# Optimization experiments

Measured on AMD Instinct MI355X. Metric: run time of the kernel, lower is better.

The kernel has to match this reference:

```python
import jax, jax.numpy as jnp
import numpy as np

B, N, C, NH = 4, 2304, 256, 8
HD = C // NH            # head dim = 32
HS = WS = 48            # H = W = sqrt(N)
RADIUS = 3.0
MLP_HID = 4 * C
SCALE = HD ** (-0.5)
NEG = -1e9              # stands in for -inf (identical softmax up to fp eps)
EPS = 1e-6


def spatial_mask():
    # get_spatial_mask: cdist of (y, x) grid coords, -inf where dist > radius
    yy, xx = jnp.meshgrid(jnp.arange(HS), jnp.arange(WS), indexing='ij')
    coords = jnp.stack([yy, xx], -1).reshape(-1, 2).astype(jnp.float32)  # [N, 2]
    d2 = jnp.sum((coords[:, None, :] - coords[None, :, :]) ** 2, -1)     # [N, N]
    return jnp.where(d2 > RADIUS * RADIUS, NEG, 0.0)


def layernorm(x, g, b):
    mu = jnp.mean(x, -1, keepdims=True)
    var = jnp.mean((x - mu) ** 2, -1, keepdims=True)
    return (x - mu) * jax.lax.rsqrt(var + EPS) * g + b


def setup_inputs() -> dict:
    key = jax.random.key(0)
    ks = jax.random.split(key, 16)
    s = 0.02
    return {
        'x':    jax.random.normal(ks[0], (B, N, C), jnp.float32),
        'x_kv': jax.random.normal(ks[1], (B, N, C), jnp.float32),
        'Wq': jax.random.normal(ks[2], (C, C), jnp.float32) * s,
        'bq': jnp.zeros((C,), jnp.float32),
        'Wk': jax.random.normal(ks[3], (C, C), jnp.float32) * s,
        'bk': jnp.zeros((C,), jnp.float32),
        'Wv': jax.random.normal(ks[4], (C, C), jnp.float32) * s,
        'bv': jnp.zeros((C,), jnp.float32),
        'Wp': jax.random.normal(ks[5], (C, C), jnp.float32) * s,
        'bp': jnp.zeros((C,), jnp.float32),
        'g1': jnp.ones((C,), jnp.float32),
        'b1': jnp.zeros((C,), jnp.float32),
        'g2': jnp.ones((C,), jnp.float32),
        'b2': jnp.zeros((C,), jnp.float32),
        'W1': jax.random.normal(ks[6], (C, MLP_HID), jnp.float32) * s,
        'bm1': jnp.zeros((MLP_HID,), jnp.float32),
        'W2': jax.random.normal(ks[7], (MLP_HID, C), jnp.float32) * s,
        'bm2': jnp.zeros((C,), jnp.float32),
    }


def reference(x, x_kv, Wq, bq, Wk, bk, Wv, bv, Wp, bp,
              g1, b1, g2, b2, W1, bm1, W2, bm2):
    mask = spatial_mask()                                  # [N, N]
    h = layernorm(x, g1, b1)
    hkv = layernorm(x_kv, g1, b1)
    q = (h @ Wq + bq).reshape(B, N, NH, HD)
    k = (hkv @ Wk + bk).reshape(B, N, NH, HD)
    v = (hkv @ Wv + bv).reshape(B, N, NH, HD)
    scores = jnp.einsum('bqhd,bkhd->bhqk', q, k) * SCALE + mask
    attn = jax.nn.softmax(scores, axis=-1)
    out = jnp.einsum('bhqk,bkhd->bqhd', attn, v).reshape(B, N, C)
    x = x + out @ Wp + bp
    m = layernorm(x, g2, b2)
    x = x + jax.nn.gelu(m @ W1 + bm1, approximate=False) @ W2 + bm2
    return x
```

## Files before the change

### kernel.cpp

```cpp
#include <hip/hip_runtime.h>
#include <hip/hip_fp16.h>
#include <math.h>

#define BB 4
#define NN 2304
#define CC 256
#define HS 48
#define HID 1024
#define BNROWS (BB * NN)
#define ATTN_SCALE 0.17677669529663687f

typedef _Float16 f16;
typedef __attribute__((ext_vector_type(2))) _Float16 h2;
typedef __attribute__((ext_vector_type(8))) _Float16 h8;
typedef __attribute__((ext_vector_type(4))) float f4;

#define GLLS16(g, l)                                                        \
    __builtin_amdgcn_global_load_lds(                                       \
        (const __attribute__((address_space(1))) unsigned int*)(g),         \
        (__attribute__((address_space(3))) unsigned int*)(l), 16, 0, 0)
#define WAIT_VM0()   asm volatile("s_waitcnt vmcnt(0)" ::: "memory")
#define WAIT_VM2()   asm volatile("s_waitcnt vmcnt(2)" ::: "memory")
#define WAIT_VM4()   asm volatile("s_waitcnt vmcnt(4)" ::: "memory")
#define WAIT_VM5()   asm volatile("s_waitcnt vmcnt(5)" ::: "memory")
#define WAIT_VM6()   asm volatile("s_waitcnt vmcnt(6)" ::: "memory")
#define WAIT_LGKM0() asm volatile("s_waitcnt lgkmcnt(0)" ::: "memory")

static __device__ __forceinline__ float wave_sum64(float v) {
    v += __shfl_xor(v, 32, 64);
    v += __shfl_xor(v, 16, 64);
    v += __shfl_xor(v, 8, 64);
    v += __shfl_xor(v, 4, 64);
    v += __shfl_xor(v, 2, 64);
    v += __shfl_xor(v, 1, 64);
    return v;
}

static __device__ __forceinline__ int xcd_swizzle_lin() {
    const int gx = (int)gridDim.x;
    const int lin = (int)blockIdx.y * gx + (int)blockIdx.x;
    const int nwg = gx * (int)gridDim.y;
    return (nwg & 7) ? lin : ((lin & 7) * (nwg >> 3) + (lin >> 3));
}

__global__ __launch_bounds__(256) void prep_ln1_kernel(
    const float* __restrict__ x, const float* __restrict__ xkv,
    const float* __restrict__ Wq, const float* __restrict__ Wk,
    const float* __restrict__ Wv, const float* __restrict__ Wp,
    const float* __restrict__ W1, const float* __restrict__ W2,
    const float* __restrict__ bq, const float* __restrict__ bk,
    const float* __restrict__ bv,
    const float* __restrict__ g, const float* __restrict__ be,
    f16* __restrict__ WqkvT, f16* __restrict__ WpT,
    f16* __restrict__ W1T, f16* __restrict__ W2T, float* __restrict__ bqkv,
    f16* __restrict__ hq, f16* __restrict__ hkv)
{
    __shared__ float tt[32][33];
    int bx = blockIdx.x;
    const int tid = threadIdx.x;
    if (bx < 768) {
        const float* src; f16* dst; int K, N;
        if (bx < 64)        { src = Wq; dst = WqkvT;           K = 256;  N = 256; }
        else if (bx < 128)  { src = Wk; dst = WqkvT + 65536;   K = 256;  N = 256;  bx -= 64; }
        else if (bx < 192)  { src = Wv; dst = WqkvT + 131072;  K = 256;  N = 256;  bx -= 128; }
        else if (bx < 256)  { src = Wp; dst = WpT;             K = 256;  N = 256;  bx -= 192; }
        else if (bx < 512)  { src = W1; dst = W1T;             K = 256;  N = 1024; bx -= 256; }
        else                { src = W2; dst = W2T;             K = 1024; N = 256;  bx -= 512; }
        const int tN = N >> 5;
        const int kt = bx / tN, nt = bx - kt * tN;
        const int rr = tid >> 5, cc = tid & 31;
#pragma unroll
        for (int j = 0; j < 4; ++j)
            tt[rr + 8 * j][cc] = src[(size_t)(kt * 32 + rr + 8 * j) * N + nt * 32 + cc];
        __syncthreads();
#pragma unroll
        for (int j = 0; j < 4; ++j)
            dst[(size_t)(nt * 32 + rr + 8 * j) * K + kt * 32 + cc] = (f16)tt[cc][rr + 8 * j];
        return;
    }
    if (bx == 768) {
        if (tid < 256) {
            bqkv[tid]       = bq[tid];
            bqkv[tid + 256] = bk[tid];
            bqkv[tid + 512] = bv[tid];
        }
        return;
    }
    const int r = (bx - 769) * 4 + (tid >> 6);
    const int lane = tid & 63;
    const float* src; f16* dst;
    if (r < BNROWS) { src = x + (size_t)r * CC;              dst = hq + (size_t)r * CC; }
    else { src = xkv + (size_t)(r - BNROWS) * CC; dst = hkv + (size_t)(r - BNROWS) * CC; }
    const float4 v = ((const float4*)src)[lane];
    const float mu = wave_sum64(v.x + v.y + v.z + v.w) * (1.0f / CC);
    const float d0 = v.x - mu, d1 = v.y - mu, d2 = v.z - mu, d3 = v.w - mu;
    const float var = wave_sum64(d0 * d0 + d1 * d1 + d2 * d2 + d3 * d3) * (1.0f / CC);
    const float rs = rsqrtf(var + 1e-6f);
    const float4 g4 = ((const float4*)g)[lane];
    const float4 b4 = ((const float4*)be)[lane];
    h2 o01 = (h2){(f16)(d0 * rs * g4.x + b4.x), (f16)(d1 * rs * g4.y + b4.y)};
    h2 o23 = (h2){(f16)(d2 * rs * g4.z + b4.z), (f16)(d3 * rs * g4.w + b4.w)};
    ((h2*)dst)[lane * 2] = o01;
    ((h2*)dst)[lane * 2 + 1] = o23;
}

template <bool QKV>
__global__ __launch_bounds__(256, 4) void gemm_wave(
    const f16* __restrict__ Aq, const f16* __restrict__ Akv,
    const f16* __restrict__ Bt, const float* __restrict__ bias,
    void* __restrict__ out1, void* __restrict__ outkv, int N, int K)
{
    __shared__ f16 lds[4 * 6144];
    const int tid = threadIdx.x;
    const int wid = tid >> 6, lane = tid & 63;
    const int ln15 = lane & 15, quad = lane >> 4;
    const int jr = lane >> 2, js = lane & 3;
    f16* slot = lds + wid * 6144;
    const int sl = xcd_swizzle_lin();
    const int gx = (int)gridDim.x;
    const int bx = sl % gx, by = sl / gx;
    const int n0 = bx * 64;
    const int m0 = (by * 4 + wid) * 32;
    const f16* Ap = QKV ? (n0 < 256 ? Aq : Akv) : Aq;

    size_t ga[2], gb[4];
#pragma unroll
    for (int i = 0; i < 2; ++i) {
        const int r = i * 16 + jr;
        const int q = (js - (r >> 1)) & 3;
        ga[i] = (size_t)(m0 + r) * K + q * 8;
    }
#pragma unroll
    for (int i = 0; i < 4; ++i) {
        const int r = i * 16 + jr;
        const int q = (js - (r >> 1)) & 3;
        gb[i] = (size_t)(n0 + r) * K + q * 8;
    }
    int aoff[2], boff[4];
#pragma unroll
    for (int mt = 0; mt < 2; ++mt) {
        const int r = mt * 16 + ln15;
        aoff[mt] = (r * 4 + ((quad + (r >> 1)) & 3)) * 16;
    }
#pragma unroll
    for (int nt = 0; nt < 4; ++nt) {
        const int r = nt * 16 + ln15;
        boff[nt] = (r * 4 + ((quad + (r >> 1)) & 3)) * 16;
    }

    f4 acc[2][4];
#pragma unroll
    for (int i = 0; i < 2; ++i)
#pragma unroll
        for (int j = 0; j < 4; ++j) acc[i][j] = (f4){0.f, 0.f, 0.f, 0.f};

    {
        f16* Al = slot;
        f16* Bl = slot + 1024;
#pragma unroll
        for (int i = 0; i < 2; ++i) GLLS16(Ap + ga[i], Al + i * 512);
#pragma unroll
        for (int i = 0; i < 4; ++i) GLLS16(Bt + gb[i], Bl + i * 512);
    }

    int cur = 0;
    for (int k0 = 0; k0 < K; k0 += 32) {
        const bool more = (k0 + 32 < K);
        f16* Ac = slot + cur * 3072;
        f16* Bc = Ac + 1024;
        if (more) {
            f16* An = slot + (cur ^ 1) * 3072;
            f16* Bn = An + 1024;
            WAIT_LGKM0();
#pragma unroll
            for (int i = 0; i < 2; ++i) GLLS16(Ap + ga[i] + k0 + 32, An + i * 512);
#pragma unroll
            for (int i = 0; i < 4; ++i) GLLS16(Bt + gb[i] + k0 + 32, Bn + i * 512);
            WAIT_VM6();
        } else {
            WAIT_VM0();
        }
        h8 aF[2], bF[4];
#pragma unroll
        for (int nt = 0; nt < 4; ++nt)
            bF[nt] = *(const h8*)((const char*)Bc + boff[nt]);
#pragma unroll
        for (int mt = 0; mt < 2; ++mt)
            aF[mt] = *(const h8*)((const char*)Ac + aoff[mt]);
#pragma unroll
        for (int mt = 0; mt < 2; ++mt)
#pragma unroll
            for (int nt = 0; nt < 4; ++nt)
                acc[mt][nt] = __builtin_amdgcn_mfma_f32_16x16x32_f16(
                    aF[mt], bF[nt], acc[mt][nt], 0, 0, 0);
        cur ^= 1;
    }

    f16* qdst = nullptr; int qstr = 0, qn0 = 0;
    if (QKV) {
        if (n0 < 256) { qdst = (f16*)out1;  qstr = 256; qn0 = n0; }
        else          { qdst = (f16*)outkv; qstr = 512; qn0 = n0 - 256; }
    }
#pragma unroll
    for (int nt = 0; nt < 4; ++nt) {
        const int gn = n0 + nt * 16 + ln15;
        const float bs = bias[gn];
#pragma unroll
        for (int mt = 0; mt < 2; ++mt) {
#pragma unroll
            for (int r = 0; r < 4; ++r) {
                const int gm = m0 + mt * 16 + quad * 4 + r;
                float v = acc[mt][nt][r] + bs;
                if (QKV) {
                    qdst[(size_t)gm * qstr + qn0 + nt * 16 + ln15] = (f16)v;
                } else {
                    ((f16*)out1)[(size_t)gm * N + gn] = (f16)v;
                }
            }
        }
    }
}

__global__ __launch_bounds__(256, 4) void gemm_op_ln2(
    const f16* __restrict__ Aa, const f16* __restrict__ Bt,
    const float* __restrict__ bias, const float* __restrict__ xres,
    const float* __restrict__ g, const float* __restrict__ be,
    f16* __restrict__ x1, f16* __restrict__ m2)
{
    __shared__ f16 lds[4 * 5120];
    __shared__ float sred[16][4][2];
    const int tid = threadIdx.x;
    const int wid = tid >> 6, lane = tid & 63;
    const int ln15 = lane & 15, quad = lane >> 4;
    const int jr = lane >> 2, js = lane & 3;
    f16* slot = lds + wid * 5120;
    const int m0 = blockIdx.x * 16;
    const int n0 = wid * 64;
    const int K = 256;

    size_t ga, gb[4];
    {
        const int q = (js - (jr >> 1)) & 3;
        ga = (size_t)(m0 + jr) * K + q * 8;
    }
#pragma unroll
    for (int i = 0; i < 4; ++i) {
        const int r = i * 16 + jr;
        const int q = (js - (r >> 1)) & 3;
        gb[i] = (size_t)(n0 + r) * K + q * 8;
    }
    const int aoff = (ln15 * 4 + ((quad + (ln15 >> 1)) & 3)) * 16;
    int boff[4];
#pragma unroll
    for (int nt = 0; nt < 4; ++nt) {
        const int r = nt * 16 + ln15;
        boff[nt] = (r * 4 + ((quad + (r >> 1)) & 3)) * 16;
    }

    f4 acc[4];
#pragma unroll
    for (int j = 0; j < 4; ++j) acc[j] = (f4){0.f, 0.f, 0.f, 0.f};

    {
        f16* Al = slot;
        f16* Bl = slot + 512;
        GLLS16(Aa + ga, Al);
#pragma unroll
        for (int i = 0; i < 4; ++i) GLLS16(Bt + gb[i], Bl + i * 512);
    }
    int cur = 0;
    for (int k0 = 0; k0 < K; k0 += 32) {
        const bool more = (k0 + 32 < K);
        f16* Ac = slot + cur * 2560;
        f16* Bc = Ac + 512;
        if (more) {
            f16* An = slot + (cur ^ 1) * 2560;
            f16* Bn = An + 512;
            WAIT_LGKM0();
            GLLS16(Aa + ga + k0 + 32, An);
#pragma unroll
            for (int i = 0; i < 4; ++i) GLLS16(Bt + gb[i] + k0 + 32, Bn + i * 512);
            WAIT_VM5();
        } else {
            WAIT_VM0();
        }
        h8 aF, bF[4];
#pragma unroll
        for (int nt = 0; nt < 4; ++nt)
            bF[nt] = *(const h8*)((const char*)Bc + boff[nt]);
        aF = *(const h8*)((const char*)Ac + aoff);
#pragma unroll
        for (int nt = 0; nt < 4; ++nt)
            acc[nt] = __builtin_amdgcn_mfma_f32_16x16x32_f16(
                aF, bF[nt], acc[nt], 0, 0, 0);
        cur ^= 1;
    }

    float bsv[4], g2v[4], b2v[4];
#pragma unroll
    for (int nt = 0; nt < 4; ++nt) {
        const int gn = n0 + nt * 16 + ln15;
        bsv[nt] = bias[gn];
        g2v[nt] = g[gn];
        b2v[nt] = be[gn];
    }
    float s1[4], s2[4];
#pragma unroll
    for (int r = 0; r < 4; ++r) { s1[r] = 0.f; s2[r] = 0.f; }
#pragma unroll
    for (int r = 0; r < 4; ++r) {
        const int gm = m0 + quad * 4 + r;
#pragma unroll
        for (int nt = 0; nt < 4; ++nt) {
            const int gn = n0 + nt * 16 + ln15;
            float v = acc[nt][r] + bsv[nt] + xres[(size_t)gm * CC + gn];
            acc[nt][r] = v;
            x1[(size_t)gm * CC + gn] = (f16)v;
            s1[r] += v;
            s2[r] += v * v;
        }
    }
#pragma unroll
    for (int off = 1; off < 16; off <<= 1) {
#pragma unroll
        for (int r = 0; r < 4; ++r) {
            s1[r] += __shfl_xor(s1[r], off, 64);
            s2[r] += __shfl_xor(s2[r], off, 64);
        }
    }
    if (ln15 == 0) {
#pragma unroll
        for (int r = 0; r < 4; ++r) {
            const int rr = quad * 4 + r;
            sred[rr][wid][0] = s1[r];
            sred[rr][wid][1] = s2[r];
        }
    }
    __syncthreads();
#pragma unroll
    for (int r = 0; r < 4; ++r) {
        const int rr = quad * 4 + r;
        const int gm = m0 + rr;
        float a = 0.f, b = 0.f;
#pragma unroll
        for (int w = 0; w < 4; ++w) {
            a += sred[rr][w][0];
            b += sred[rr][w][1];
        }
        const float mu = a * (1.0f / CC);
        const float var = fmaxf(b * (1.0f / CC) - mu * mu, 0.0f);
        const float rs = rsqrtf(var + 1e-6f);
#pragma unroll
        for (int nt = 0; nt < 4; ++nt) {
            const int gn = n0 + nt * 16 + ln15;
            const float v = acc[nt][r];
            m2[(size_t)gm * CC + gn] = (f16)((v - mu) * rs * g2v[nt] + b2v[nt]);
        }
    }
}

template <int BM, int BN, int WGM, int WGN, bool GELU, bool FINAL>
__global__ __launch_bounds__(256, 2) void gemm_pipe(
    const f16* __restrict__ A, const f16* __restrict__ Bt,
    const float* __restrict__ bias, const f16* __restrict__ resid16,
    void* __restrict__ outv, int N, int K)
{
    constexpr int A_G = BM / 16, B_G = BN / 16, T = A_G + B_G;
    constexpr int L = T / 4;
    constexpr int BUFE = (BM + BN) * 32;
    constexpr int WM = BM / WGM, WN = BN / WGN;
    constexpr int MT = WM / 16;
    static_assert(WN == 64, "epilogue assumes 4 n-frags of 16");
    static_assert(T % 4 == 0, "stage loads divide across 4 waves");
    __shared__ f16 lds[3 * BUFE];
    const int tid = threadIdx.x;
    const int wid = tid >> 6, lane = tid & 63;
    const int ln15 = lane & 15, quad = lane >> 4;
    const int jr = lane >> 2, js = lane & 3;
    const int wr = wid / WGN, wc = wid % WGN;

    const int sl = xcd_swizzle_lin();
    const int gx = (int)gridDim.x;
    const int m0 = (sl % gx) * BM;
    const int n0 = (sl / gx) * BN;

    const size_t gabase = (size_t)jr * K + (size_t)(((js - (jr >> 1)) & 3) * 8);

    int aoff[MT], boff[4];
#pragma unroll
    for (int mt = 0; mt < MT; ++mt) {
        const int rr = wr * WM + mt * 16 + ln15;
        aoff[mt] = (rr * 4 + ((quad + (rr >> 1)) & 3)) * 16;
    }
#pragma unroll
    for (int nt = 0; nt < 4; ++nt) {
        const int rr = wc * WN + nt * 16 + ln15;
        boff[nt] = BM * 64 + (rr * 4 + ((quad + (rr >> 1)) & 3)) * 16;
    }

    f4 acc[MT][4];
#pragma unroll
    for (int i = 0; i < MT; ++i)
#pragma unroll
        for (int j = 0; j < 4; ++j) acc[i][j] = (f4){0.f, 0.f, 0.f, 0.f};

#define GP_STAGE(dst, kk)                                                     \
    _Pragma("unroll")                                                         \
    for (int i = 0; i < L; ++i) {                                             \
        const int g = wid + i * 4;                                            \
        const f16* base;                                                      \
        int dofs;                                                             \
        if (g < A_G) {                                                        \
            base = A + (size_t)(m0 + g * 16) * K;                             \
            dofs = g * 512;                                                   \
        } else {                                                              \
            base = Bt + (size_t)(n0 + (g - A_G) * 16) * K;                    \
            dofs = BM * 32 + (g - A_G) * 512;                                 \
        }                                                                     \
        GLLS16(base + gabase + (kk), (dst) + dofs);                           \
    }

    GP_STAGE(lds, 0);
    GP_STAGE(lds + BUFE, 32);

    const int nst = K >> 5;
    for (int s = 0; s < nst; ++s) {
        if (s + 1 < nst) {
            if constexpr (L == 4) { WAIT_VM4(); } else { WAIT_VM2(); }
        } else {
            WAIT_VM0();
        }
        __builtin_amdgcn_s_barrier();
        __builtin_amdgcn_sched_barrier(0);
        if (s + 2 < nst) { GP_STAGE(lds + ((s + 2) % 3) * BUFE, (s + 2) * 32); }
        f16* bufc = lds + (s % 3) * BUFE;
        h8 aF[MT], bF[4];
#pragma unroll
        for (int nt = 0; nt < 4; ++nt)
            bF[nt] = *(const h8*)((const char*)bufc + boff[nt]);
#pragma unroll
        for (int mt = 0; mt < MT; ++mt)
            aF[mt] = *(const h8*)((const char*)bufc + aoff[mt]);
        __builtin_amdgcn_s_setprio(1);
#pragma unroll
        for (int mt = 0; mt < MT; ++mt)
#pragma unroll
            for (int nt = 0; nt < 4; ++nt)
                acc[mt][nt] = __builtin_amdgcn_mfma_f32_16x16x32_f16(
                    aF[mt], bF[nt], acc[mt][nt], 0, 0, 0);
        __builtin_amdgcn_s_setprio(0);
    }
#undef GP_STAGE

#pragma unroll
    for (int nt = 0; nt < 4; ++nt) {
        const int gn = n0 + wc * WN + nt * 16 + ln15;
        const float bs = bias[gn];
#pragma unroll
        for (int mt = 0; mt < MT; ++mt) {
#pragma unroll
            for (int r = 0; r < 4; ++r) {
                const int gm = m0 + wr * WM + mt * 16 + quad * 4 + r;
                float v = acc[mt][nt][r] + bs;
                if (GELU) v = 0.5f * v * (1.0f + erff(v * 0.70710678118654752f));
                if (FINAL) {
                    v += (float)resid16[(size_t)gm * N + gn];
                    ((float*)outv)[(size_t)gm * N + gn] = v;
                } else {
                    ((f16*)outv)[(size_t)gm * N + gn] = (f16)v;
                }
            }
        }
    }
}

__device__ __constant__ int ATT_DY[29] = {
    -3, -2, -2, -2, -2, -2, -1, -1, -1, -1, -1, 0, 0, 0, 0,
    0, 0, 0, 1, 1, 1, 1, 1, 2, 2, 2, 2, 2, 3};
__device__ __constant__ int ATT_DX[29] = {
    0, -2, -1, 0, 1, 2, -2, -1, 0, 1, 2, -3, -2, -1, 0,
    1, 2, 3, -2, -1, 0, 1, 2, -2, -1, 0, 1, 2, 0};

__global__ __launch_bounds__(128) void attn_tile_kernel(
    const f16* __restrict__ qf, const f16* __restrict__ kvf,
    f16* __restrict__ ao)
{
    __shared__ f16 ks[196][66];
    __shared__ f16 vs[196][66];
    const int tile = blockIdx.x, hp = blockIdx.y, b = blockIdx.z;
    const int ty0 = (tile / 6) * 8, tx0 = (tile - (tile / 6) * 6) * 8;
    const int tid = threadIdx.x;

    const int q = tid & 63, hh = tid >> 6;
    const int qy = q >> 3, qx = q & 7;
    const size_t qrow = (size_t)b * NN + (ty0 + qy) * HS + tx0 + qx;
    const f16* qp = qf + qrow * CC + hp * 64 + hh * 32;
    uint4 qa[4];
#pragma unroll
    for (int i = 0; i < 4; ++i) qa[i] = ((const uint4*)qp)[i];

#pragma unroll
    for (int bt = 0; bt < 5; ++bt) {
        uint4 v[5];
        int rr[5], sg[5];
#pragma unroll
        for (int j = 0; j < 5; ++j) {
            const int it = bt * 5 + j;
            const int idx = tid + it * 128;
            const int r = idx >> 4, seg = idx & 15;
            rr[j] = r; sg[j] = seg;
            const int ry = r / 14;
            const int gy = ty0 - 3 + ry, gx = tx0 - 3 + (r - ry * 14);
            uint4 val = {0u, 0u, 0u, 0u};
            const bool act = (it < 24) || (tid < 64);
            if (act && (unsigned)gy < HS && (unsigned)gx < HS) {
                const size_t rowb = ((size_t)b * NN + gy * HS + gx) * 512;
                const int ch = (seg < 8) ? (hp * 64 + seg * 8)
                                         : (256 + hp * 64 + (seg - 8) * 8);
                val = *(const uint4*)&kvf[rowb + ch];
            }
            v[j] = val;
        }
#pragma unroll
        for (int j = 0; j < 5; ++j) {
            const int it = bt * 5 + j;
            if (it == 24 && tid >= 64) continue;
            f16* dstp = (sg[j] < 8) ? &ks[rr[j]][(sg[j] & 7) * 8]
                                    : &vs[rr[j]][(sg[j] & 7) * 8];
            ((unsigned int*)dstp)[0] = v[j].x;
            ((unsigned int*)dstp)[1] = v[j].y;
            ((unsigned int*)dstp)[2] = v[j].z;
            ((unsigned int*)dstp)[3] = v[j].w;
        }
    }
    __syncthreads();

    const h2* q2 = (const h2*)qa;

    float s[29];
#pragma unroll
    for (int n = 0; n < 29; ++n) {
        const int dy = ATT_DY[n], dx = ATT_DX[n];
        const int r = (qy + 3 + dy) * 14 + qx + 3 + dx;
        const bool valid = (unsigned)(ty0 + qy + dy) < HS &&
                           (unsigned)(tx0 + qx + dx) < HS;
        float a = 0.0f;
        const h2* kp = (const h2*)&ks[r][hh * 32];
#pragma unroll
        for (int i = 0; i < 16; ++i)
            a = __builtin_amdgcn_fdot2(q2[i], kp[i], a, false);
        s[n] = valid ? a * ATTN_SCALE : -1e30f;
    }
    float m = s[0];
#pragma unroll
    for (int n = 1; n < 29; ++n) m = fmaxf(m, s[n]);
    float l = 0.0f;
#pragma unroll
    for (int n = 0; n < 29; ++n) { s[n] = __expf(s[n] - m); l += s[n]; }
    h2 a2[16];
#pragma unroll
    for (int i = 0; i < 16; ++i) a2[i] = (h2){(f16)0.f, (f16)0.f};
#pragma unroll
    for (int n = 0; n < 29; ++n) {
        const int dy = ATT_DY[n], dx = ATT_DX[n];
        const int r = (qy + 3 + dy) * 14 + qx + 3 + dx;
        const f16 pn = (f16)s[n];
        const h2 ph = (h2){pn, pn};
        const h2* vp = (const h2*)&vs[r][hh * 32];
#pragma unroll
        for (int i = 0; i < 16; ++i) a2[i] += ph * vp[i];
    }
    const float inv = 1.0f / l;
    uint4 ov[4];
    f16* oh = (f16*)ov;
#pragma unroll
    for (int i = 0; i < 16; ++i) {
        oh[2 * i]     = (f16)((float)a2[i][0] * inv);
        oh[2 * i + 1] = (f16)((float)a2[i][1] * inv);
    }
    uint4* dst = (uint4*)(ao + qrow * CC + hp * 64 + hh * 32);
#pragma unroll
    for (int i = 0; i < 4; ++i) dst[i] = ov[i];
}

extern "C" void kernel_launch(void* const* d_in, const int* in_sizes, int n_in,
                              void* d_out, int out_size, void* d_ws, size_t ws_size,
                              hipStream_t stream) {
    const float* x    = (const float*)d_in[0];
    const float* x_kv = (const float*)d_in[1];
    const float* Wq   = (const float*)d_in[2];
    const float* bq   = (const float*)d_in[3];
    const float* Wk   = (const float*)d_in[4];
    const float* bk   = (const float*)d_in[5];
    const float* Wv   = (const float*)d_in[6];
    const float* bv   = (const float*)d_in[7];
    const float* Wp   = (const float*)d_in[8];
    const float* bp   = (const float*)d_in[9];
    const float* g1   = (const float*)d_in[10];
    const float* b1   = (const float*)d_in[11];
    const float* g2   = (const float*)d_in[12];
    const float* b2   = (const float*)d_in[13];
    const float* W1   = (const float*)d_in[14];
    const float* bm1  = (const float*)d_in[15];
    const float* W2   = (const float*)d_in[16];
    const float* bm2  = (const float*)d_in[17];
    float* outp = (float*)d_out;

    f16* wsh = (f16*)d_ws;
    f16* WqkvT = wsh;
    f16* WpT   = wsh + 196608;
    f16* W1T   = wsh + 262144;
    f16* W2T   = wsh + 524288;
    float* bqkv = (float*)(wsh + 786432);
    f16* hq    = wsh + 787968;
    f16* hkv   = wsh + 3147264;
    f16* qf    = wsh + 5506560;
    f16* kvf   = wsh + 7865856;
    f16* ao    = hq;
    f16* x1    = hkv;
    f16* m2    = qf;
    f16* hidF  = kvf;
    const bool fused = ws_size >= (size_t)17303040 * sizeof(f16);

    prep_ln1_kernel<<<5377, 256, 0, stream>>>(
        x, x_kv, Wq, Wk, Wv, Wp, W1, W2, bq, bk, bv, g1, b1,
        WqkvT, WpT, W1T, W2T, bqkv, hq, hkv);
    gemm_wave<true><<<dim3(12, 72), 256, 0, stream>>>(
        hq, hkv, WqkvT, bqkv, qf, kvf, 768, 256);
    attn_tile_kernel<<<dim3(36, 4, BB), 128, 0, stream>>>(qf, kvf, ao);
    gemm_op_ln2<<<576, 256, 0, stream>>>(ao, WpT, bp, x, g2, b2, x1, m2);
    if (fused) {
        gemm_pipe<128, 128, 2, 2, true, false>
            <<<dim3(72, 8), 256, 0, stream>>>(
                m2, W1T, bm1, nullptr, hidF, HID, 256);
        gemm_pipe<64, 64, 4, 1, false, true>
            <<<dim3(144, 4), 256, 0, stream>>>(
                hidF, W2T, bm2, x1, outp, CC, 1024);
    } else {
        for (int b = 0; b < BB; ++b) {
            const size_t off = (size_t)b * NN * CC;
            gemm_pipe<128, 128, 2, 2, true, false>
                <<<dim3(18, 8), 256, 0, stream>>>(
                    m2 + off, W1T, bm1, nullptr, hidF, HID, 256);
            gemm_pipe<64, 64, 4, 1, false, true>
                <<<dim3(36, 4), 256, 0, stream>>>(
                    hidF, W2T, bm2, x1 + off, outp + off, CC, 1024);
        }
    }
    (void)in_sizes; (void)n_in; (void)out_size;
}
```

Baseline: 177.9 us.

## Fuse out-proj+LN2, MLP up and MLP down into one persistent kernel

Replaces three separate launches (out-projection with LN2, GELU MLP-up GEMM, MLP-down GEMM) with one persistent 512-block kernel that loops over tiles and separates the phases with software grid barriers built on global atomic counters. The counters are zeroed in the prep kernel. The aim is to remove launch gaps and the tail idle time between the three kernels. In exchange it relies on all 512 blocks being co-resident, since otherwise the spin barrier deadlocks. The barrier adds fence and atomic polling cost, and the fixed grid gives uneven tile counts per block (576 tiles over 512 blocks).

```diff
diff --git a/kernel.cpp b/kernel.cpp
--- a/kernel.cpp
+++ b/kernel.cpp
@@ -43,6 +43,23 @@
     return (nwg & 7) ? lin : ((lin & 7) * (nwg >> 3) + (lin >> 3));
 }
 
+static __device__ __forceinline__ void sw_gbar(unsigned* ctr, unsigned target) {
+    __threadfence();
+    __syncthreads();
+    if (threadIdx.x == 0) {
+        __hip_atomic_fetch_add(ctr, 1u, __ATOMIC_ACQ_REL,
+                               __HIP_MEMORY_SCOPE_AGENT);
+        unsigned v;
+        do {
+            __builtin_amdgcn_s_sleep(2);
+            v = __hip_atomic_load(ctr, __ATOMIC_ACQUIRE,
+                                  __HIP_MEMORY_SCOPE_AGENT);
+        } while (v < target);
+    }
+    __syncthreads();
+    __threadfence();
+}
+
 __global__ __launch_bounds__(256) void prep_ln1_kernel(
     const float* __restrict__ x, const float* __restrict__ xkv,
     const float* __restrict__ Wq, const float* __restrict__ Wk,
@@ -53,7 +70,7 @@
     const float* __restrict__ g, const float* __restrict__ be,
     f16* __restrict__ WqkvT, f16* __restrict__ WpT,
     f16* __restrict__ W1T, f16* __restrict__ W2T, float* __restrict__ bqkv,
-    f16* __restrict__ hq, f16* __restrict__ hkv)
+    f16* __restrict__ hq, f16* __restrict__ hkv, unsigned* gctr)
 {
     __shared__ float tt[32][33];
     int bx = blockIdx.x;
@@ -84,6 +101,9 @@
             bqkv[tid + 256] = bk[tid];
             bqkv[tid + 512] = bv[tid];
         }
+        if (gctr && tid < 8)
+            __hip_atomic_store(&gctr[tid], 0u, __ATOMIC_RELEASE,
+                               __HIP_MEMORY_SCOPE_AGENT);
         return;
     }
     const int r = (bx - 769) * 4 + (tid >> 6);
@@ -221,20 +241,18 @@
     }
 }
 
-__global__ __launch_bounds__(256, 4) void gemm_op_ln2(
+static __device__ __forceinline__ void opln2_body(
     const f16* __restrict__ Aa, const f16* __restrict__ Bt,
     const float* __restrict__ bias, const float* __restrict__ xres,
     const float* __restrict__ g, const float* __restrict__ be,
-    f16* __restrict__ x1, f16* __restrict__ m2)
+    f16* __restrict__ x1, f16* __restrict__ m2, int m0, f16* ldsb,
+    float (*sred)[4][2])
 {
-    __shared__ f16 lds[4 * 5120];
-    __shared__ float sred[16][4][2];
     const int tid = threadIdx.x;
     const int wid = tid >> 6, lane = tid & 63;
     const int ln15 = lane & 15, quad = lane >> 4;
     const int jr = lane >> 2, js = lane & 3;
-    f16* slot = lds + wid * 5120;
-    const int m0 = blockIdx.x * 16;
+    f16* slot = ldsb + wid * 5120;
     const int n0 = wid * 64;
     const int K = 256;
 
@@ -360,10 +378,10 @@
 }
 
 template <int BM, int BN, int WGM, int WGN, bool GELU, bool FINAL>
-__global__ __launch_bounds__(256, 2) void gemm_pipe(
+static __device__ __forceinline__ void pipe_body(
     const f16* __restrict__ A, const f16* __restrict__ Bt,
     const float* __restrict__ bias, const f16* __restrict__ resid16,
-    void* __restrict__ outv, int N, int K)
+    void* __restrict__ outv, int N, int K, int m0, int n0, f16* lds)
 {
     constexpr int A_G = BM / 16, B_G = BN / 16, T = A_G + B_G;
     constexpr int L = T / 4;
@@ -372,17 +390,11 @@
     constexpr int MT = WM / 16;
     static_assert(WN == 64, "epilogue assumes 4 n-frags of 16");
     static_assert(T % 4 == 0, "stage loads divide across 4 waves");
-    __shared__ f16 lds[3 * BUFE];
     const int tid = threadIdx.x;
     const int wid = tid >> 6, lane = tid & 63;
     const int ln15 = lane & 15, quad = lane >> 4;
     const int jr = lane >> 2, js = lane & 3;
     const int wr = wid / WGN, wc = wid % WGN;
-
-    const int sl = xcd_swizzle_lin();
-    const int gx = (int)gridDim.x;
-    const int m0 = (sl % gx) * BM;
-    const int n0 = (sl / gx) * BN;
 
     const size_t gabase = (size_t)jr * K + (size_t)(((js - (jr >> 1)) & 3) * 8);
 
@@ -471,6 +483,69 @@
                 }
             }
         }
+    }
+}
+
+__global__ __launch_bounds__(256, 4) void gemm_op_ln2(
+    const f16* __restrict__ Aa, const f16* __restrict__ Bt,
+    const float* __restrict__ bias, const float* __restrict__ xres,
+    const float* __restrict__ g, const float* __restrict__ be,
+    f16* __restrict__ x1, f16* __restrict__ m2)
+{
+    __shared__ f16 lds[4 * 5120];
+    __shared__ float sred[16][4][2];
+    opln2_body(Aa, Bt, bias, xres, g, be, x1, m2, blockIdx.x * 16, lds, sred);
+}
+
+template <int BM, int BN, int WGM, int WGN, bool GELU, bool FINAL>
+__global__ __launch_bounds__(256, 2) void gemm_pipe(
+    const f16* __restrict__ A, const f16* __restrict__ Bt,
+    const float* __restrict__ bias, const f16* __restrict__ resid16,
+    void* __restrict__ outv, int N, int K)
+{
+    __shared__ f16 lds[3 * (BM + BN) * 32];
+    const int sl = xcd_swizzle_lin();
+    const int gx = (int)gridDim.x;
+    pipe_body<BM, BN, WGM, WGN, GELU, FINAL>(
+        A, Bt, bias, resid16, outv, N, K, (sl % gx) * BM, (sl / gx) * BN, lds);
+}
+
+__global__ __launch_bounds__(256, 2) void tail3_kernel(
+    const f16* __restrict__ ao, const f16* __restrict__ WpT,
+    const float* __restrict__ bp, const float* __restrict__ x,
+    const float* __restrict__ g2, const float* __restrict__ b2,
+    f16* __restrict__ x1, f16* __restrict__ m2,
+    const f16* __restrict__ W1T, const float* __restrict__ bm1,
+    f16* __restrict__ hidF, const f16* __restrict__ W2T,
+    const float* __restrict__ bm2, float* __restrict__ outp,
+    unsigned* __restrict__ gctr)
+{
+    __shared__ f16 smem[24576];
+    __shared__ float sred[16][4][2];
+    const int bid = (int)blockIdx.x;
+    const unsigned nb = gridDim.x;
+
+    for (int j = bid; j < 576; j += (int)nb) {
+        opln2_body(ao, WpT, bp, x, g2, b2, x1, m2, j * 16, smem, sred);
+        __syncthreads();
+    }
+    sw_gbar(&gctr[0], nb);
+
+    for (int j = bid; j < 576; j += (int)nb) {
+        const int sl = (j & 7) * 72 + (j >> 3);
+        pipe_body<128, 128, 2, 2, true, false>(
+            m2, W1T, bm1, nullptr, hidF, HID, 256,
+            (sl % 72) * 128, (sl / 72) * 128, smem);
+        __syncthreads();
+    }
+    sw_gbar(&gctr[1], nb);
+
+    for (int j = bid; j < 576; j += (int)nb) {
+        const int sl = (j & 7) * 72 + (j >> 3);
+        pipe_body<64, 64, 4, 1, false, true>(
+            hidF, W2T, bm2, x1, outp, CC, 1024,
+            (sl % 144) * 64, (sl / 144) * 64, smem);
+        __syncthreads();
     }
 }
 
@@ -620,23 +695,21 @@
     f16* x1    = hkv;
     f16* m2    = qf;
     f16* hidF  = kvf;
-    const bool fused = ws_size >= (size_t)17303040 * sizeof(f16);
+    unsigned* gctr = (unsigned*)(wsh + 17303040);
+    const bool fused = ws_size >= (size_t)17303040 * sizeof(f16) + 256;
 
     prep_ln1_kernel<<<5377, 256, 0, stream>>>(
         x, x_kv, Wq, Wk, Wv, Wp, W1, W2, bq, bk, bv, g1, b1,
-        WqkvT, WpT, W1T, W2T, bqkv, hq, hkv);
+        WqkvT, WpT, W1T, W2T, bqkv, hq, hkv, fused ? gctr : nullptr);
     gemm_wave<true><<<dim3(12, 72), 256, 0, stream>>>(
         hq, hkv, WqkvT, bqkv, qf, kvf, 768, 256);
     attn_tile_kernel<<<dim3(36, 4, BB), 128, 0, stream>>>(qf, kvf, ao);
-    gemm_op_ln2<<<576, 256, 0, stream>>>(ao, WpT, bp, x, g2, b2, x1, m2);
     if (fused) {
-        gemm_pipe<128, 128, 2, 2, true, false>
-            <<<dim3(72, 8), 256, 0, stream>>>(
-                m2, W1T, bm1, nullptr, hidF, HID, 256);
-        gemm_pipe<64, 64, 4, 1, false, true>
-            <<<dim3(144, 4), 256, 0, stream>>>(
-                hidF, W2T, bm2, x1, outp, CC, 1024);
+        tail3_kernel<<<512, 256, 0, stream>>>(
+            ao, WpT, bp, x, g2, b2, x1, m2,
+            W1T, bm1, hidF, W2T, bm2, outp, gctr);
     } else {
+        gemm_op_ln2<<<576, 256, 0, stream>>>(ao, WpT, bp, x, g2, b2, x1, m2);
         for (int b = 0; b < BB; ++b) {
             const size_t off = (size_t)b * NN * CC;
             gemm_pipe<128, 128, 2, 2, true, false>
```

Result: slower. 506.9 us (+184.9%).
